# Kernel optimization log

Hardware: AMD Instinct MI355X
Metric: run time of the kernel (lower is better)

Reference implementation:

```python
import jax, jax.numpy as jnp
import numpy as np

B, L, D_T, DH, ALPHA, DTE, H, NL, DFF = 256, 64, 768, 128, 48, 64, 8, 3, 512


def setup_inputs() -> dict:
    key = jax.random.key(0)
    ks = jax.random.split(key, 24)
    n = lambda i, shape, s=1.0: jax.random.normal(ks[i], shape, dtype=jnp.float32) * s
    return {
        "cls_emb": n(0, (B, L, D_T)),
        "note_times": jnp.sort(jax.random.uniform(ks[1], (B, L), dtype=jnp.float32) * 48.0, axis=-1),
        "note_counts": jax.random.randint(ks[2], (B,), 1, L + 1).astype(jnp.int32),
        "proj_w": n(3, (D_T, DH), D_T ** -0.5), "proj_b": jnp.zeros((DH,), jnp.float32),
        "te_w": n(4, (DTE,)), "te_b": n(5, (DTE,)),
        "wq": n(6, (DTE, DTE), DTE ** -0.5), "wk": n(7, (DTE, DTE), DTE ** -0.5),
        "tf_wq": n(8, (NL, DH, DH), DH ** -0.5), "tf_wk": n(9, (NL, DH, DH), DH ** -0.5),
        "tf_wv": n(10, (NL, DH, DH), DH ** -0.5), "tf_wo": n(11, (NL, DH, DH), DH ** -0.5),
        "tf_ln1_g": jnp.ones((NL, DH), jnp.float32), "tf_ln1_b": jnp.zeros((NL, DH), jnp.float32),
        "tf_w1": n(12, (NL, DH, DFF), DH ** -0.5), "tf_b1": jnp.zeros((NL, DFF), jnp.float32),
        "tf_w2": n(13, (NL, DFF, DH), DFF ** -0.5), "tf_b2": jnp.zeros((NL, DH), jnp.float32),
        "tf_ln2_g": jnp.ones((NL, DH), jnp.float32), "tf_ln2_b": jnp.zeros((NL, DH), jnp.float32),
        "cls_w1": n(14, (DH, DH // 2), DH ** -0.5), "cls_b1": jnp.zeros((DH // 2,), jnp.float32),
        "cls_w2": n(15, (DH // 2, 1), (DH // 2) ** -0.5), "cls_b2": jnp.zeros((1,), jnp.float32),
    }


def _ln(x, g, b):
    mu = x.mean(-1, keepdims=True)
    var = x.var(-1, keepdims=True)
    return (x - mu) * jax.lax.rsqrt(var + 1e-5) * g + b


def _time_embed(t, w, b):
    # mTAND time embedding: dim 0 linear, rest periodic (sin)
    lin = t[..., None] * w + b
    return jnp.concatenate([lin[..., :1], jnp.sin(lin[..., 1:])], axis=-1)


def _forward(cls_emb, note_times, note_counts, proj_w, proj_b, te_w, te_b, wq, wk,
             tf_wq, tf_wk, tf_wv, tf_wo, tf_ln1_g, tf_ln1_b, tf_w1, tf_b1,
             tf_w2, tf_b2, tf_ln2_g, tf_ln2_b, cls_w1, cls_b1, cls_w2, cls_b2):
    # project frozen Longformer CLS embeddings -> note embeddings [B, L, DH]
    note_emb = cls_emb @ proj_w + proj_b
    alpha_pts = jnp.arange(ALPHA, dtype=jnp.float32)
    q_te = _time_embed(alpha_pts, te_w, te_b)          # [A, DTE]
    k_te = _time_embed(note_times, te_w, te_b)         # [B, L, DTE]
    dk = DTE // H
    q = (q_te @ wq).reshape(ALPHA, H, dk)
    k = (k_te @ wk).reshape(B, L, H, dk)
    scores = jnp.einsum('ahd,blhd->bhal', q, k) / np.float32(np.sqrt(dk))
    valid = jnp.arange(L)[None, :] < note_counts[:, None]      # [B, L] ragged mask
    scores = jnp.where(valid[:, None, None, :], scores, jnp.float32(-1e9))
    attn = jax.nn.softmax(scores, axis=-1)                     # [B, H, A, L]
    # one batched interpolation replaces the per-patient / per-dim python loops
    x = jnp.einsum('bhal,blf->bahf', attn, note_emb).mean(axis=2)  # [B, A, DH]
    x = jnp.where((note_counts > 0)[:, None, None], x, 0.0)
    # 3-layer post-norm transformer encoder over the alpha time grid
    hd = DH // H
    for i in range(NL):
        qh = (x @ tf_wq[i]).reshape(B, ALPHA, H, hd)
        kh = (x @ tf_wk[i]).reshape(B, ALPHA, H, hd)
        vh = (x @ tf_wv[i]).reshape(B, ALPHA, H, hd)
        s = jnp.einsum('bqhd,bkhd->bhqk', qh, kh) / np.float32(np.sqrt(hd))
        a = jax.nn.softmax(s, axis=-1)
        o = jnp.einsum('bhqk,bkhd->bqhd', a, vh).reshape(B, ALPHA, DH) @ tf_wo[i]
        x = _ln(x + o, tf_ln1_g[i], tf_ln1_b[i])
        f = jax.nn.relu(x @ tf_w1[i] + tf_b1[i]) @ tf_w2[i] + tf_b2[i]
        x = _ln(x + f, tf_ln2_g[i], tf_ln2_b[i])
    last = x[:, -1, :]
    logits = jax.nn.relu(last @ cls_w1 + cls_b1) @ cls_w2 + cls_b2
    return logits


def reference(cls_emb, note_times, note_counts, proj_w, proj_b, te_w, te_b, wq, wk,
              tf_wq, tf_wk, tf_wv, tf_wo, tf_ln1_g, tf_ln1_b, tf_w1, tf_b1,
              tf_w2, tf_b2, tf_ln2_g, tf_ln2_b, cls_w1, cls_b1, cls_w2, cls_b2):
    return _forward(cls_emb, note_times, note_counts, proj_w, proj_b, te_w, te_b, wq, wk,
                    tf_wq, tf_wk, tf_wv, tf_wo, tf_ln1_g, tf_ln1_b, tf_w1, tf_b1,
                    tf_w2, tf_b2, tf_ln2_g, tf_ln2_b, cls_w1, cls_b1, cls_w2, cls_b2)
```

## Files before the change

### kernel.cpp

```cpp
#include <hip/hip_runtime.h>
#include <hip/hip_bf16.h>

#define B_   256
#define L_   64
#define DT_  768
#define DH_  128
#define AL_  48
#define DTE_ 64
#define H_   8
#define NL_  3
#define DFF_ 512

typedef __attribute__((ext_vector_type(4))) float f32x4;
typedef __attribute__((ext_vector_type(4))) unsigned int u32x4;
typedef __attribute__((ext_vector_type(2))) unsigned int u32x2;
typedef __attribute__((ext_vector_type(8))) short short8;

__device__ inline unsigned short f2bf(float f) {
    union { float f; unsigned u; } v; v.f = f;
    unsigned r = (v.u + 0x7FFFu + ((v.u >> 16) & 1u)) >> 16;
    return (unsigned short)r;
}
__device__ inline unsigned f2bf2(float a, float b) {
    return (unsigned)f2bf(a) | ((unsigned)f2bf(b) << 16);
}
__device__ inline float bf2f(unsigned short u) {
    union { unsigned u; float f; } v; v.u = ((unsigned)u) << 16; return v.f;
}
__device__ inline short8 ldg8(const unsigned short* p) {
    union { short8 s; u32x4 v; } r;
    r.v = *(const u32x4*)p;
    return r.s;
}
__device__ inline unsigned pk_f16(float a, float b) {
    unsigned r;
    asm("v_cvt_pkrtz_f16_f32 %0, %1, %2" : "=v"(r) : "v"(a), "v"(b));
    return r;
}
__device__ inline unsigned pk_max(unsigned a, unsigned b) {
    unsigned r;
    asm("v_pk_max_f16 %0, %1, %2" : "=v"(r) : "v"(a), "v"(b));
    return r;
}
__device__ inline float f16_lo(unsigned h) {
    float f; asm("v_cvt_f32_f16 %0, %1" : "=v"(f) : "v"(h)); return f;
}
__device__ inline float f16_hi(unsigned h) {
    float f; unsigned t = h >> 16;
    asm("v_cvt_f32_f16 %0, %1" : "=v"(f) : "v"(t)); return f;
}

struct TEnt { const float* src; int dstOff; int K; int N; int tile0; };
struct TTab { TEnt e[19]; };

__global__ __launch_bounds__(256) void prep_weights_kernel(
    TTab tab, int ntile, unsigned short* __restrict__ wt,
    const float* __restrict__ te_w, const float* __restrict__ te_b,
    const float* __restrict__ wq, float* __restrict__ q_allG)
{
    __shared__ unsigned short lds[64][72];
    __shared__ float qte[AL_ * 68];
    int tid = threadIdx.x;
    if ((int)blockIdx.x >= ntile) {
        for (int i = tid; i < AL_ * 64; i += 256) {
            int a = i >> 6, j = i & 63;
            float lin = fmaf((float)a, te_w[j], te_b[j]);
            qte[a * 68 + j] = (j == 0) ? lin : __sinf(lin);
        }
        __syncthreads();
        for (int i = tid; i < AL_ * 64; i += 256) {
            int a = i >> 6, d = i & 63;
            float s0 = 0.f, s1 = 0.f, s2 = 0.f, s3 = 0.f;
            for (int j = 0; j < 64; j += 4) {
                s0 = fmaf(qte[a * 68 + j],     wq[j * 64 + d],       s0);
                s1 = fmaf(qte[a * 68 + j + 1], wq[(j + 1) * 64 + d], s1);
                s2 = fmaf(qte[a * 68 + j + 2], wq[(j + 2) * 64 + d], s2);
                s3 = fmaf(qte[a * 68 + j + 3], wq[(j + 3) * 64 + d], s3);
            }
            q_allG[i] = (s0 + s1) + (s2 + s3);
        }
        return;
    }
    int ei = 0;
    #pragma unroll
    for (int j = 1; j < 19; ++j) if ((int)blockIdx.x >= tab.e[j].tile0) ei = j;
    TEnt e = tab.e[ei];
    int t = blockIdx.x - e.tile0;
    int tilesK = e.K >> 6;
    int tk = t % tilesK, tn = t / tilesK;
    #pragma unroll
    for (int p = 0; p < 16; ++p) {
        int kk = p * 4 + (tid >> 6);
        int n = tid & 63;
        float v = e.src[(size_t)(tk * 64 + kk) * e.N + tn * 64 + n];
        lds[n][kk] = f2bf(v);
    }
    __syncthreads();
    #pragma unroll
    for (int p = 0; p < 2; ++p) {
        int c = p * 256 + tid;
        int n = c >> 3, q = c & 7;
        u32x4 v = *(const u32x4*)(&lds[n][q * 8]);
        *(u32x4*)(&wt[(size_t)e.dstOff + (size_t)(tn * 64 + n) * e.K + tk * 64 + q * 8]) = v;
    }
}

__global__ __launch_bounds__(256) void gemm_proj_kernel(
    const float* __restrict__ A, const unsigned short* __restrict__ Wt,
    const float* __restrict__ bias, unsigned short* __restrict__ C,
    int M, int N, int K)
{
    __shared__ unsigned short As[32 * 64];
    __shared__ unsigned short Bs[128 * 64];
    int tid = threadIdx.x;
    int bm = blockIdx.x * 32;
    int wave = tid >> 6, lane = tid & 63;
    int wm = wave >> 1, wn = wave & 1;
    int g = lane >> 4, r16 = lane & 15;

    f32x4 acc[4] = {};

    for (int k0 = 0; k0 < K; k0 += 64) {
        #pragma unroll
        for (int p = 0; p < 2; ++p) {
            int row = p * 16 + (tid >> 4);
            int c4 = tid & 15;
            f32x4 v = *(const f32x4*)(&A[(size_t)(bm + row) * K + k0 + c4 * 4]);
            u32x2 w;
            w[0] = f2bf2(v[0], v[1]);
            w[1] = f2bf2(v[2], v[3]);
            *(u32x2*)(&As[row * 64 + ((c4 * 4) ^ ((row & 7) << 3))]) = w;
        }
        #pragma unroll
        for (int p = 0; p < 4; ++p) {
            int c = p * 256 + tid;
            int n = c >> 3, q = c & 7;
            u32x4 v = *(const u32x4*)(&Wt[(size_t)n * K + k0 + q * 8]);
            *(u32x4*)(&Bs[n * 64 + ((q * 8) ^ ((n & 7) << 3))]) = v;
        }
        __syncthreads();
        #pragma unroll
        for (int kk = 0; kk < 2; ++kk) {
            short8 af, bf[4];
            int co = kk * 32 + g * 8;
            {
                int row = wm * 16 + r16;
                af = *(const short8*)(&As[row * 64 + (co ^ ((row & 7) << 3))]);
            }
            #pragma unroll
            for (int ni = 0; ni < 4; ++ni) {
                int row = wn * 64 + ni * 16 + r16;
                bf[ni] = *(const short8*)(&Bs[row * 64 + (co ^ ((row & 7) << 3))]);
            }
            #pragma unroll
            for (int ni = 0; ni < 4; ++ni)
                acc[ni] = __builtin_amdgcn_mfma_f32_16x16x32_bf16(af, bf[ni], acc[ni], 0, 0, 0);
        }
        __syncthreads();
    }
    #pragma unroll
    for (int ni = 0; ni < 4; ++ni) {
        int col = wn * 64 + ni * 16 + r16;
        float bv = bias[col];
        #pragma unroll
        for (int r = 0; r < 4; ++r) {
            int row = bm + wm * 16 + g * 4 + r;
            C[(size_t)row * N + col] = f2bf(acc[ni][r] + bv);
        }
    }
}

__global__ __launch_bounds__(256) void first_attn_kernel(
    const float* __restrict__ note_times, const int* __restrict__ note_counts,
    const float* __restrict__ te_w, const float* __restrict__ te_b,
    const float* __restrict__ wk, const float* __restrict__ q_all,
    const unsigned short* __restrict__ note_emb,
    float* __restrict__ x_out, unsigned short* __restrict__ xbf_out)
{
    __shared__ union RU {
        float kkL[64 * 68];
        unsigned short E[32 * 256];
        struct { unsigned short As[32 * 64]; unsigned short Bs[128 * 64]; } mm;
    } ru;
    __shared__ float rsL[32][8];

    const int bx = blockIdx.x;
    const int b = bx >> 1, a0 = (bx & 1) * 24;
    const int tid = threadIdx.x, lane = tid & 63;
    const int wv = __builtin_amdgcn_readfirstlane(tid >> 6);
    const int g = lane >> 4, r16 = lane & 15;
    const int nc = note_counts[b];

    float kte[64];
    {
        float t = note_times[b * 64 + lane];
        #pragma unroll
        for (int j = 0; j < 64; ++j) {
            float lin = fmaf(t, te_w[j], te_b[j]);
            kte[j] = (j == 0) ? lin : __sinf(lin);
        }
    }
    {
        float kvp[16] = {};
        #pragma unroll
        for (int j = 0; j < 64; ++j) {
            #pragma unroll
            for (int dd = 0; dd < 16; ++dd)
                kvp[dd] = fmaf(kte[j], wk[j * 64 + wv * 16 + dd], kvp[dd]);
        }
        #pragma unroll
        for (int q4 = 0; q4 < 4; ++q4)
            *(f32x4*)(&ru.kkL[lane * 68 + wv * 16 + q4 * 4]) = *(const f32x4*)(&kvp[q4 * 4]);
    }
    __syncthreads();
    float kv[64];
    #pragma unroll
    for (int q4 = 0; q4 < 16; ++q4)
        *(f32x4*)(&kv[q4 * 4]) = *(const f32x4*)(&ru.kkL[lane * 68 + q4 * 4]);
    __syncthreads();

    float abar[6] = {};
    const float scale = 0.35355339059327373f;
    #pragma unroll
    for (int p = 0; p < 2; ++p) {
        float e_reg[6][4];
        #pragma unroll
        for (int i = 0; i < 6; ++i) {
            int a = wv * 6 + i;
            float s[4];
            #pragma unroll
            for (int h = 0; h < 4; ++h) {
                float acc = 0.f;
                #pragma unroll
                for (int d = 0; d < 8; ++d)
                    acc = fmaf(q_all[(a0 + a) * 64 + p * 32 + h * 8 + d],
                               kv[p * 32 + h * 8 + d], acc);
                s[h] = (lane < nc) ? acc * scale : -1e9f;
            }
            unsigned m0 = pk_f16(s[0], s[1]);
            unsigned m1 = pk_f16(s[2], s[3]);
            #pragma unroll
            for (int st = 32; st >= 1; st >>= 1) {
                m0 = pk_max(m0, (unsigned)__shfl_xor((int)m0, st));
                m1 = pk_max(m1, (unsigned)__shfl_xor((int)m1, st));
            }
            float mm[4] = { f16_lo(m0), f16_hi(m0), f16_lo(m1), f16_hi(m1) };
            #pragma unroll
            for (int h = 0; h < 4; ++h) {
                float e = __expf(s[h] - mm[h]);
                e_reg[i][h] = e;
                int k = h * 64 + lane;
                ru.E[a * 256 + (k ^ ((a & 7) << 3))] = f2bf(e);
            }
        }
        __syncthreads();
        if (wv < 2) {
            f32x4 acc = {0.f, 0.f, 0.f, 0.f};
            #pragma unroll
            for (int ks = 0; ks < 8; ++ks) {
                int row = wv * 16 + r16;
                short8 af = *(const short8*)(&ru.E[row * 256 + ((ks * 32 + g * 8) ^ ((row & 7) << 3))]);
                short bb = (r16 == (ks >> 1)) ? (short)0x3F80 : (short)0;
                short8 bf = { bb, bb, bb, bb, bb, bb, bb, bb };
                acc = __builtin_amdgcn_mfma_f32_16x16x32_bf16(af, bf, acc, 0, 0, 0);
            }
            if (r16 < 4) {
                #pragma unroll
                for (int r = 0; r < 4; ++r)
                    rsL[wv * 16 + g * 4 + r][p * 4 + r16] = 0.125f / fmaxf(acc[r], 1e-20f);
            }
        }
        __syncthreads();
        #pragma unroll
        for (int i = 0; i < 6; ++i) {
            int a = wv * 6 + i;
            f32x4 rv = *(const f32x4*)(&rsL[a][p * 4]);
            abar[i] = fmaf(e_reg[i][0], rv[0], abar[i]);
            abar[i] = fmaf(e_reg[i][1], rv[1], abar[i]);
            abar[i] = fmaf(e_reg[i][2], rv[2], abar[i]);
            abar[i] = fmaf(e_reg[i][3], rv[3], abar[i]);
        }
    }
    {
        int l = tid & 63;
        #pragma unroll
        for (int pp = 0; pp < 4; ++pp) {
            int c = pp * 4 + (tid >> 6);
            u32x4 v = *(const u32x4*)(&note_emb[((size_t)b * 64 + l) * 128 + c * 8]);
            #pragma unroll
            for (int j = 0; j < 8; ++j) {
                unsigned short h16 = (unsigned short)((j & 1) ? (v[j >> 1] >> 16) : (v[j >> 1] & 0xffff));
                int f = c * 8 + j;
                ru.mm.Bs[f * 64 + (l ^ ((f & 7) << 3))] = h16;
            }
        }
    }
    #pragma unroll
    for (int i = 0; i < 6; ++i) {
        int a = wv * 6 + i;
        ru.mm.As[a * 64 + (lane ^ ((a & 7) << 3))] = f2bf(abar[i]);
    }
    __syncthreads();

    f32x4 pv[4] = {};
    #pragma unroll
    for (int q = 0; q < 4; ++q) {
        int f = wv * 4 + q, mi = f >> 3, ni = f & 7;
        #pragma unroll
        for (int ks = 0; ks < 2; ++ks) {
            int co = ks * 32 + g * 8;
            int raw = mi * 16 + r16, rb = ni * 16 + r16;
            short8 af = *(const short8*)(&ru.mm.As[raw * 64 + (co ^ ((raw & 7) << 3))]);
            short8 bf = *(const short8*)(&ru.mm.Bs[rb * 64 + (co ^ ((rb & 7) << 3))]);
            pv[q] = __builtin_amdgcn_mfma_f32_16x16x32_bf16(af, bf, pv[q], 0, 0, 0);
        }
    }
    #pragma unroll
    for (int q = 0; q < 4; ++q) {
        int f = wv * 4 + q, mi = f >> 3, ni = f & 7;
        #pragma unroll
        for (int r = 0; r < 4; ++r) {
            int row = mi * 16 + g * 4 + r;
            if (row < 24) {
                float v = (nc > 0) ? pv[q][r] : 0.f;
                size_t o = ((size_t)b * AL_ + a0 + row) * 128 + ni * 16 + r16;
                x_out[o] = v;
                xbf_out[o] = f2bf(v);
            }
        }
    }
}

__global__ __launch_bounds__(192) void attn2_kernel(
    const unsigned short* __restrict__ xbf, const unsigned short* __restrict__ WtL,
    unsigned short* __restrict__ o)
{
    __shared__ unsigned short Xs[AL_ * 128];
    __shared__ unsigned short qM[AL_ * 40];
    __shared__ unsigned short kM[AL_ * 40];
    __shared__ unsigned short vT[16 * 72];
    __shared__ float sL[AL_ * 52];
    __shared__ unsigned short P[AL_ * 64];
    int bid = blockIdx.x;
    int b = bid >> 3, h = bid & 7;
    int tid = threadIdx.x, lane = tid & 63;
    int wv = __builtin_amdgcn_readfirstlane(tid >> 6);
    int g = lane >> 4, r16 = lane & 15;

    #pragma unroll
    for (int p = 0; p < 4; ++p) {
        int i = p * 192 + tid;
        int a = i >> 4, c = (i & 15) * 8;
        u32x4 v = *(const u32x4*)(&xbf[((size_t)b * AL_ + a) * 128 + c]);
        *(u32x4*)(&Xs[a * 128 + (c & 64) + ((c & 63) ^ ((a & 7) << 3))]) = v;
    }
    for (int i = tid; i < 768; i += 192) {
        int a = i >> 4, k2 = 16 + (i & 15);
        qM[a * 40 + k2] = 0;
        kM[a * 40 + k2] = 0;
    }
    for (int i = tid; i < 256; i += 192) {
        int d = i >> 4, k2 = 48 + (i & 15);
        vT[d * 72 + k2] = 0;
    }
    for (int i = tid; i < 768; i += 192) {
        int a = i >> 4, c = 48 + (i & 15);
        P[a * 64 + (c ^ ((a & 7) << 3))] = 0;
    }
    __syncthreads();

    {
        f32x4 acc[3] = {};
        const unsigned short* Wm = WtL + wv * 16384 + (size_t)(h * 16) * 128;
        #pragma unroll
        for (int kq = 0; kq < 4; ++kq) {
            short8 bf = ldg8(&Wm[(size_t)r16 * 128 + kq * 32 + g * 8]);
            #pragma unroll
            for (int mi = 0; mi < 3; ++mi) {
                int row = mi * 16 + r16;
                int c = kq * 32 + g * 8;
                short8 af = *(const short8*)(&Xs[row * 128 + (c & 64) + ((c & 63) ^ ((row & 7) << 3))]);
                acc[mi] = __builtin_amdgcn_mfma_f32_16x16x32_bf16(af, bf, acc[mi], 0, 0, 0);
            }
        }
        #pragma unroll
        for (int mi = 0; mi < 3; ++mi) {
            #pragma unroll
            for (int r = 0; r < 4; ++r) {
                int a = mi * 16 + g * 4 + r;
                unsigned short hv = f2bf(acc[mi][r]);
                if (wv == 0) qM[a * 40 + r16] = hv;
                else if (wv == 1) kM[a * 40 + r16] = hv;
                else vT[r16 * 72 + a] = hv;
            }
        }
    }
    __syncthreads();

    {
        #pragma unroll
        for (int ni = 0; ni < 3; ++ni) {
            f32x4 acc = {0.f, 0.f, 0.f, 0.f};
            short8 af = *(const short8*)(&qM[(wv * 16 + r16) * 40 + g * 8]);
            short8 bf = *(const short8*)(&kM[(ni * 16 + r16) * 40 + g * 8]);
            acc = __builtin_amdgcn_mfma_f32_16x16x32_bf16(af, bf, acc, 0, 0, 0);
            #pragma unroll
            for (int r = 0; r < 4; ++r)
                sL[(wv * 16 + g * 4 + r) * 52 + ni * 16 + r16] = acc[r] * 0.25f;
        }
    }
    __syncthreads();

    {
        int row = wv * 16 + (lane >> 2), sub = lane & 3;
        f32x4 v0 = *(const f32x4*)(&sL[row * 52 + sub * 4]);
        f32x4 v1 = *(const f32x4*)(&sL[row * 52 + 16 + sub * 4]);
        f32x4 v2 = *(const f32x4*)(&sL[row * 52 + 32 + sub * 4]);
        float m = fmaxf(fmaxf(fmaxf(v0[0], v0[1]), fmaxf(v0[2], v0[3])),
                        fmaxf(fmaxf(v1[0], v1[1]), fmaxf(v1[2], v1[3])));
        m = fmaxf(m, fmaxf(fmaxf(v2[0], v2[1]), fmaxf(v2[2], v2[3])));
        m = fmaxf(m, __shfl_xor(m, 1));
        m = fmaxf(m, __shfl_xor(m, 2));
        float e[12];
        #pragma unroll
        for (int j = 0; j < 4; ++j) {
            e[j]     = __expf(v0[j] - m);
            e[4 + j] = __expf(v1[j] - m);
            e[8 + j] = __expf(v2[j] - m);
        }
        float sum = 0.f;
        #pragma unroll
        for (int j = 0; j < 12; ++j) sum += e[j];
        sum += __shfl_xor(sum, 1);
        sum += __shfl_xor(sum, 2);
        float inv = __fdividef(1.f, sum);
        #pragma unroll
        for (int c = 0; c < 3; ++c) {
            u32x2 w;
            w[0] = f2bf2(e[c * 4 + 0] * inv, e[c * 4 + 1] * inv);
            w[1] = f2bf2(e[c * 4 + 2] * inv, e[c * 4 + 3] * inv);
            int col = c * 16 + sub * 4;
            *(u32x2*)(&P[row * 64 + (col ^ ((row & 7) << 3))]) = w;
        }
    }
    __syncthreads();

    {
        f32x4 acc = {0.f, 0.f, 0.f, 0.f};
        #pragma unroll
        for (int ks = 0; ks < 2; ++ks) {
            int co = ks * 32 + g * 8;
            int rp = wv * 16 + r16;
            short8 af = *(const short8*)(&P[rp * 64 + (co ^ ((rp & 7) << 3))]);
            short8 bf = *(const short8*)(&vT[r16 * 72 + co]);
            acc = __builtin_amdgcn_mfma_f32_16x16x32_bf16(af, bf, acc, 0, 0, 0);
        }
        #pragma unroll
        for (int r = 0; r < 4; ++r) {
            int a = wv * 16 + g * 4 + r;
            o[((size_t)b * AL_ + a) * 128 + h * 16 + r16] = f2bf(acc[r]);
        }
    }
}

__global__ __launch_bounds__(256) void layer_tail_kernel(
    const unsigned short* __restrict__ obuf, const unsigned short* __restrict__ Wl,
    const float* __restrict__ b1, const float* __restrict__ b2,
    const float* __restrict__ g1, const float* __restrict__ be1,
    const float* __restrict__ g2, const float* __restrict__ be2,
    float* __restrict__ x, unsigned short* __restrict__ xbf,
    int last, const float* __restrict__ cw1, const float* __restrict__ cb1,
    const float* __restrict__ cw2, const float* __restrict__ cb2,
    float* __restrict__ outp)
{
    __shared__ unsigned short OX[16 * 128];
    __shared__ union { unsigned short hid[16 * 512]; float Cs[16 * 132]; } u2;
    __shared__ float xr[16 * 132];
    const int tid = threadIdx.x, lane = tid & 63;
    const int wv = __builtin_amdgcn_readfirstlane(tid >> 6);
    const int g = lane >> 4, r16 = lane & 15;
    const int row0 = last ? ((int)blockIdx.x * 48 + 32) : ((int)blockIdx.x * 16);

    {
        int a = tid >> 4, c = (tid & 15) * 8;
        u32x4 v = *(const u32x4*)(&obuf[(size_t)(row0 + a) * 128 + c]);
        *(u32x4*)(&OX[a * 128 + (c & 64) + ((c & 63) ^ ((a & 7) << 3))]) = v;
    }
    __syncthreads();

    {
        f32x4 wacc[2] = {};
        #pragma unroll
        for (int q = 0; q < 2; ++q) {
            int ni = wv * 2 + q;
            const unsigned short* Wm = Wl + 49152 + (size_t)(ni * 16 + r16) * 128;
            #pragma unroll
            for (int kq = 0; kq < 4; ++kq) {
                int co = kq * 32 + g * 8;
                short8 af = *(const short8*)(&OX[r16 * 128 + (co & 64) + ((co & 63) ^ ((r16 & 7) << 3))]);
                short8 bf = ldg8(Wm + co);
                wacc[q] = __builtin_amdgcn_mfma_f32_16x16x32_bf16(af, bf, wacc[q], 0, 0, 0);
            }
        }
        #pragma unroll
        for (int q = 0; q < 2; ++q) {
            int ni = wv * 2 + q;
            #pragma unroll
            for (int r = 0; r < 4; ++r)
                u2.Cs[(g * 4 + r) * 132 + ni * 16 + r16] = wacc[q][r];
        }
    }
    __syncthreads();

    #pragma unroll
    for (int rr = 0; rr < 4; ++rr) {
        int row = wv * 4 + rr;
        size_t go = (size_t)(row0 + row) * 128;
        float v0 = u2.Cs[row * 132 + lane] + x[go + lane];
        float v1 = u2.Cs[row * 132 + 64 + lane] + x[go + 64 + lane];
        float sum = v0 + v1, sq = v0 * v0 + v1 * v1;
        #pragma unroll
        for (int o2 = 32; o2 >= 1; o2 >>= 1) {
            sum += __shfl_xor(sum, o2);
            sq  += __shfl_xor(sq, o2);
        }
        float mu = sum * (1.f / 128.f);
        float var = sq * (1.f / 128.f) - mu * mu;
        float rs = rsqrtf(var + 1e-5f);
        float o0 = (v0 - mu) * rs * g1[lane] + be1[lane];
        float o1 = (v1 - mu) * rs * g1[lane + 64] + be1[lane + 64];
        xr[row * 132 + lane] = o0;
        xr[row * 132 + 64 + lane] = o1;
        OX[row * 128 + (lane ^ ((row & 7) << 3))] = f2bf(o0);
        OX[row * 128 + 64 + (lane ^ ((row & 7) << 3))] = f2bf(o1);
    }
    __syncthreads();

    {
        f32x4 hacc[8] = {};
        #pragma unroll
        for (int nf = 0; nf < 8; ++nf) {
            int col = wv * 128 + nf * 16 + r16;
            const unsigned short* Wm = Wl + 65536 + (size_t)col * 128;
            #pragma unroll
            for (int kq = 0; kq < 4; ++kq) {
                int co = kq * 32 + g * 8;
                short8 bf = ldg8(Wm + co);
                short8 af = *(const short8*)(&OX[r16 * 128 + (co & 64) + ((co & 63) ^ ((r16 & 7) << 3))]);
                hacc[nf] = __builtin_amdgcn_mfma_f32_16x16x32_bf16(af, bf, hacc[nf], 0, 0, 0);
            }
        }
        #pragma unroll
        for (int nf = 0; nf < 8; ++nf) {
            int col = wv * 128 + nf * 16 + r16;
            float bv = b1[col];
            #pragma unroll
            for (int r = 0; r < 4; ++r) {
                int rowa = g * 4 + r;
                u2.hid[rowa * 512 + (col & 448) + ((col & 63) ^ ((rowa & 7) << 3))] =
                    f2bf(fmaxf(hacc[nf][r] + bv, 0.f));
            }
        }
    }
    __syncthreads();

    f32x4 yacc[2] = {};
    #pragma unroll
    for (int q = 0; q < 2; ++q) {
        int ni = wv * 2 + q;
        const unsigned short* Wm = Wl + 131072 + (size_t)(ni * 16 + r16) * 512;
        #pragma unroll
        for (int kq = 0; kq < 16; ++kq) {
            int co = kq * 32 + g * 8;
            short8 af = *(const short8*)(&u2.hid[r16 * 512 + (co & 448) + ((co & 63) ^ ((r16 & 7) << 3))]);
            short8 bf = ldg8(Wm + co);
            yacc[q] = __builtin_amdgcn_mfma_f32_16x16x32_bf16(af, bf, yacc[q], 0, 0, 0);
        }
    }
    __syncthreads();
    #pragma unroll
    for (int q = 0; q < 2; ++q) {
        int ni = wv * 2 + q;
        float bv = b2[ni * 16 + r16];
        #pragma unroll
        for (int r = 0; r < 4; ++r)
            u2.Cs[(g * 4 + r) * 132 + ni * 16 + r16] = yacc[q][r] + bv;
    }
    __syncthreads();

    #pragma unroll
    for (int rr = 0; rr < 4; ++rr) {
        int row = wv * 4 + rr;
        size_t go = (size_t)(row0 + row) * 128;
        float v0 = u2.Cs[row * 132 + lane] + xr[row * 132 + lane];
        float v1 = u2.Cs[row * 132 + 64 + lane] + xr[row * 132 + 64 + lane];
        float sum = v0 + v1, sq = v0 * v0 + v1 * v1;
        #pragma unroll
        for (int o2 = 32; o2 >= 1; o2 >>= 1) {
            sum += __shfl_xor(sum, o2);
            sq  += __shfl_xor(sq, o2);
        }
        float mu = sum * (1.f / 128.f);
        float var = sq * (1.f / 128.f) - mu * mu;
        float rs = rsqrtf(var + 1e-5f);
        float o0 = (v0 - mu) * rs * g2[lane] + be2[lane];
        float o1 = (v1 - mu) * rs * g2[lane + 64] + be2[lane + 64];
        if (!last) {
            x[go + lane] = o0;
            x[go + 64 + lane] = o1;
            xbf[go + lane] = f2bf(o0);
            xbf[go + 64 + lane] = f2bf(o1);
        } else {
            xr[row * 132 + lane] = o0;
            xr[row * 132 + 64 + lane] = o1;
        }
    }
    if (last) {
        __syncthreads();
        if (wv == 0) {
            float hj = cb1[lane];
            #pragma unroll 8
            for (int d = 0; d < 128; ++d)
                hj = fmaf(xr[15 * 132 + d], cw1[d * 64 + lane], hj);
            hj = fmaxf(hj, 0.f);
            float acc = hj * cw2[lane];
            #pragma unroll
            for (int o2 = 32; o2 >= 1; o2 >>= 1) acc += __shfl_xor(acc, o2);
            if (lane == 0) outp[blockIdx.x] = acc + cb2[0];
        }
    }
}

extern "C" void kernel_launch(void* const* d_in, const int* in_sizes, int n_in,
                              void* d_out, int out_size, void* d_ws, size_t ws_size,
                              hipStream_t stream) {
    (void)in_sizes; (void)n_in; (void)out_size; (void)ws_size;
    const float* cls_emb    = (const float*)d_in[0];
    const float* note_times = (const float*)d_in[1];
    const int*   note_counts= (const int*)d_in[2];
    const float* proj_w     = (const float*)d_in[3];
    const float* proj_b     = (const float*)d_in[4];
    const float* te_w       = (const float*)d_in[5];
    const float* te_b       = (const float*)d_in[6];
    const float* wq         = (const float*)d_in[7];
    const float* wk         = (const float*)d_in[8];
    const float* tf_wq      = (const float*)d_in[9];
    const float* tf_wk      = (const float*)d_in[10];
    const float* tf_wv      = (const float*)d_in[11];
    const float* tf_wo      = (const float*)d_in[12];
    const float* tf_ln1_g   = (const float*)d_in[13];
    const float* tf_ln1_b   = (const float*)d_in[14];
    const float* tf_w1      = (const float*)d_in[15];
    const float* tf_b1      = (const float*)d_in[16];
    const float* tf_w2      = (const float*)d_in[17];
    const float* tf_b2      = (const float*)d_in[18];
    const float* tf_ln2_g   = (const float*)d_in[19];
    const float* tf_ln2_b   = (const float*)d_in[20];
    const float* cls_w1     = (const float*)d_in[21];
    const float* cls_b1     = (const float*)d_in[22];
    const float* cls_w2     = (const float*)d_in[23];
    const float* cls_b2     = (const float*)d_in[24];
    float* out = (float*)d_out;
    float* ws = (float*)d_ws;

    unsigned short* note_emb16 = (unsigned short*)(ws + 0);
    float* x        = ws + 1048576;
    unsigned short* obuf16 = (unsigned short*)(ws + 2621440);
    unsigned short* xbf    = (unsigned short*)(ws + 3407872);
    float* q_all    = ws + 4194304;
    unsigned short* wt     = (unsigned short*)(ws + 4197376);

    TTab tab;
    int tile = 0, idx = 0;
    auto add = [&](const float* src, int dstOff, int K, int N) {
        tab.e[idx].src = src; tab.e[idx].dstOff = dstOff;
        tab.e[idx].K = K; tab.e[idx].N = N; tab.e[idx].tile0 = tile;
        tile += (K / 64) * (N / 64); ++idx;
    };
    add(proj_w, 0, DT_, DH_);
    int layerBase[NL_];
    for (int i = 0; i < NL_; ++i) {
        int base = 98304 + i * 196608;
        layerBase[i] = base;
        add(tf_wq + (size_t)i * DH_ * DH_, base,           DH_, DH_);
        add(tf_wk + (size_t)i * DH_ * DH_, base + 16384,   DH_, DH_);
        add(tf_wv + (size_t)i * DH_ * DH_, base + 32768,   DH_, DH_);
        add(tf_wo + (size_t)i * DH_ * DH_, base + 49152,   DH_, DH_);
        add(tf_w1 + (size_t)i * DH_ * DFF_, base + 65536,  DH_, DFF_);
        add(tf_w2 + (size_t)i * DFF_ * DH_, base + 131072, DFF_, DH_);
    }
    prep_weights_kernel<<<tile + 1, 256, 0, stream>>>(tab, tile, wt, te_w, te_b, wq, q_all);

    const int Mx = B_ * AL_;

    gemm_proj_kernel<<<(B_ * L_) / 32, 256, 0, stream>>>(
        cls_emb, wt, proj_b, note_emb16, B_ * L_, DH_, DT_);

    first_attn_kernel<<<B_ * 2, 256, 0, stream>>>(
        note_times, note_counts, te_w, te_b, wk, q_all, note_emb16, x, xbf);

    for (int i = 0; i < NL_; ++i) {
        int base = layerBase[i];
        int last = (i == NL_ - 1);
        attn2_kernel<<<B_ * H_, 192, 0, stream>>>(xbf, wt + base, obuf16);
        layer_tail_kernel<<<last ? B_ : (Mx / 16), 256, 0, stream>>>(
            obuf16, wt + base,
            tf_b1 + i * DFF_, tf_b2 + i * DH_,
            tf_ln1_g + i * DH_, tf_ln1_b + i * DH_,
            tf_ln2_g + i * DH_, tf_ln2_b + i * DH_,
            x, xbf,
            last, cls_w1, cls_b1, cls_w2, cls_b2, out);
    }
}
```

Before: 187.5 us.

## Process 32 rows per layer-tail block and alias attention shared buffers

The layer tail kernel is templated on the number of rows per block. Non-final layers now use 32-row tiles, so each loaded weight fragment feeds two MFMA row tiles and global weight traffic per row is halved. The attention kernel overlays its shared buffers through unions: X with the score buffer, and the q/k buffers with P, with P's zero padding moved to after the softmax. This is meant to cut LDS footprint and raise occupancy, at the cost of more registers and fewer blocks in the tail kernel.

After: 174.0 us. 1.08x faster.

```diff
diff --git a/kernel.cpp b/kernel.cpp
--- a/kernel.cpp
+++ b/kernel.cpp
@@ -335,12 +335,15 @@
     const unsigned short* __restrict__ xbf, const unsigned short* __restrict__ WtL,
     unsigned short* __restrict__ o)
 {
-    __shared__ unsigned short Xs[AL_ * 128];
-    __shared__ unsigned short qM[AL_ * 40];
-    __shared__ unsigned short kM[AL_ * 40];
+    __shared__ union UA {
+        unsigned short Xs[AL_ * 128];
+        float sL[AL_ * 52];
+    } ua;
+    __shared__ union UB {
+        struct { unsigned short qM[AL_ * 40]; unsigned short kM[AL_ * 40]; } qk;
+        unsigned short P[AL_ * 64];
+    } ub;
     __shared__ unsigned short vT[16 * 72];
-    __shared__ float sL[AL_ * 52];
-    __shared__ unsigned short P[AL_ * 64];
     int bid = blockIdx.x;
     int b = bid >> 3, h = bid & 7;
     int tid = threadIdx.x, lane = tid & 63;
@@ -352,21 +355,17 @@
         int i = p * 192 + tid;
         int a = i >> 4, c = (i & 15) * 8;
         u32x4 v = *(const u32x4*)(&xbf[((size_t)b * AL_ + a) * 128 + c]);
-        *(u32x4*)(&Xs[a * 128 + (c & 64) + ((c & 63) ^ ((a & 7) << 3))]) = v;
+        *(u32x4*)(&ua.Xs[a * 128 + (c & 64) + ((c & 63) ^ ((a & 7) << 3))]) = v;
     }
     for (int i = tid; i < 768; i += 192) {
         int a = i >> 4, k2 = 16 + (i & 15);
-        qM[a * 40 + k2] = 0;
-        kM[a * 40 + k2] = 0;
+        ub.qk.qM[a * 40 + k2] = 0;
+        ub.qk.kM[a * 40 + k2] = 0;
     }
     for (int i = tid; i < 256; i += 192) {
         int d = i >> 4, k2 = 48 + (i & 15);
         vT[d * 72 + k2] = 0;
     }
-    for (int i = tid; i < 768; i += 192) {
-        int a = i >> 4, c = 48 + (i & 15);
-        P[a * 64 + (c ^ ((a & 7) << 3))] = 0;
-    }
     __syncthreads();
 
     {
@@ -379,7 +378,7 @@
             for (int mi = 0; mi < 3; ++mi) {
                 int row = mi * 16 + r16;
                 int c = kq * 32 + g * 8;
-                short8 af = *(const short8*)(&Xs[row * 128 + (c & 64) + ((c & 63) ^ ((row & 7) << 3))]);
+                short8 af = *(const short8*)(&ua.Xs[row * 128 + (c & 64) + ((c & 63) ^ ((row & 7) << 3))]);
                 acc[mi] = __builtin_amdgcn_mfma_f32_16x16x32_bf16(af, bf, acc[mi], 0, 0, 0);
             }
         }
@@ -389,8 +388,8 @@
             for (int r = 0; r < 4; ++r) {
                 int a = mi * 16 + g * 4 + r;
                 unsigned short hv = f2bf(acc[mi][r]);
-                if (wv == 0) qM[a * 40 + r16] = hv;
-                else if (wv == 1) kM[a * 40 + r16] = hv;
+                if (wv == 0) ub.qk.qM[a * 40 + r16] = hv;
+                else if (wv == 1) ub.qk.kM[a * 40 + r16] = hv;
                 else vT[r16 * 72 + a] = hv;
             }
         }
@@ -401,21 +400,21 @@
         #pragma unroll
         for (int ni = 0; ni < 3; ++ni) {
             f32x4 acc = {0.f, 0.f, 0.f, 0.f};
-            short8 af = *(const short8*)(&qM[(wv * 16 + r16) * 40 + g * 8]);
-            short8 bf = *(const short8*)(&kM[(ni * 16 + r16) * 40 + g * 8]);
+            short8 af = *(const short8*)(&ub.qk.qM[(wv * 16 + r16) * 40 + g * 8]);
+            short8 bf = *(const short8*)(&ub.qk.kM[(ni * 16 + r16) * 40 + g * 8]);
             acc = __builtin_amdgcn_mfma_f32_16x16x32_bf16(af, bf, acc, 0, 0, 0);
             #pragma unroll
             for (int r = 0; r < 4; ++r)
-                sL[(wv * 16 + g * 4 + r) * 52 + ni * 16 + r16] = acc[r] * 0.25f;
+                ua.sL[(wv * 16 + g * 4 + r) * 52 + ni * 16 + r16] = acc[r] * 0.25f;
         }
     }
     __syncthreads();
 
     {
         int row = wv * 16 + (lane >> 2), sub = lane & 3;
-        f32x4 v0 = *(const f32x4*)(&sL[row * 52 + sub * 4]);
-        f32x4 v1 = *(const f32x4*)(&sL[row * 52 + 16 + sub * 4]);
-        f32x4 v2 = *(const f32x4*)(&sL[row * 52 + 32 + sub * 4]);
+        f32x4 v0 = *(const f32x4*)(&ua.sL[row * 52 + sub * 4]);
+        f32x4 v1 = *(const f32x4*)(&ua.sL[row * 52 + 16 + sub * 4]);
+        f32x4 v2 = *(const f32x4*)(&ua.sL[row * 52 + 32 + sub * 4]);
         float m = fmaxf(fmaxf(fmaxf(v0[0], v0[1]), fmaxf(v0[2], v0[3])),
                         fmaxf(fmaxf(v1[0], v1[1]), fmaxf(v1[2], v1[3])));
         m = fmaxf(m, fmaxf(fmaxf(v2[0], v2[1]), fmaxf(v2[2], v2[3])));
@@ -440,7 +439,11 @@
             w[0] = f2bf2(e[c * 4 + 0] * inv, e[c * 4 + 1] * inv);
             w[1] = f2bf2(e[c * 4 + 2] * inv, e[c * 4 + 3] * inv);
             int col = c * 16 + sub * 4;
-            *(u32x2*)(&P[row * 64 + (col ^ ((row & 7) << 3))]) = w;
+            *(u32x2*)(&ub.P[row * 64 + (col ^ ((row & 7) << 3))]) = w;
+        }
+        for (int i = tid; i < 768; i += 192) {
+            int a = i >> 4, c = 48 + (i & 15);
+            ub.P[a * 64 + (c ^ ((a & 7) << 3))] = 0;
         }
     }
     __syncthreads();
@@ -451,7 +454,7 @@
         for (int ks = 0; ks < 2; ++ks) {
             int co = ks * 32 + g * 8;
             int rp = wv * 16 + r16;
-            short8 af = *(const short8*)(&P[rp * 64 + (co ^ ((rp & 7) << 3))]);
+            short8 af = *(const short8*)(&ub.P[rp * 64 + (co ^ ((rp & 7) << 3))]);
             short8 bf = *(const short8*)(&vT[r16 * 72 + co]);
             acc = __builtin_amdgcn_mfma_f32_16x16x32_bf16(af, bf, acc, 0, 0, 0);
         }
@@ -463,6 +466,7 @@
     }
 }
 
+template<int ROWS>
 __global__ __launch_bounds__(256) void layer_tail_kernel(
     const unsigned short* __restrict__ obuf, const unsigned short* __restrict__ Wl,
     const float* __restrict__ b1, const float* __restrict__ b2,
@@ -473,23 +477,26 @@
     const float* __restrict__ cw2, const float* __restrict__ cb2,
     float* __restrict__ outp)
 {
-    __shared__ unsigned short OX[16 * 128];
-    __shared__ union { unsigned short hid[16 * 512]; float Cs[16 * 132]; } u2;
-    __shared__ float xr[16 * 132];
+    constexpr int MR = ROWS / 16;
+    __shared__ unsigned short OX[ROWS * 128];
+    __shared__ union { unsigned short hid[ROWS * 512]; float Cs[ROWS * 132]; } u2;
+    __shared__ float xr[ROWS * 132];
     const int tid = threadIdx.x, lane = tid & 63;
     const int wv = __builtin_amdgcn_readfirstlane(tid >> 6);
     const int g = lane >> 4, r16 = lane & 15;
-    const int row0 = last ? ((int)blockIdx.x * 48 + 32) : ((int)blockIdx.x * 16);
-
-    {
-        int a = tid >> 4, c = (tid & 15) * 8;
+    const int row0 = last ? ((int)blockIdx.x * 48 + 32) : ((int)blockIdx.x * ROWS);
+
+    #pragma unroll
+    for (int p = 0; p < MR; ++p) {
+        int i = p * 256 + tid;
+        int a = i >> 4, c = (i & 15) * 8;
         u32x4 v = *(const u32x4*)(&obuf[(size_t)(row0 + a) * 128 + c]);
         *(u32x4*)(&OX[a * 128 + (c & 64) + ((c & 63) ^ ((a & 7) << 3))]) = v;
     }
     __syncthreads();
 
     {
-        f32x4 wacc[2] = {};
+        f32x4 wacc[MR][2] = {};
         #pragma unroll
         for (int q = 0; q < 2; ++q) {
             int ni = wv * 2 + q;
@@ -497,24 +504,30 @@
             #pragma unroll
             for (int kq = 0; kq < 4; ++kq) {
                 int co = kq * 32 + g * 8;
-                short8 af = *(const short8*)(&OX[r16 * 128 + (co & 64) + ((co & 63) ^ ((r16 & 7) << 3))]);
                 short8 bf = ldg8(Wm + co);
-                wacc[q] = __builtin_amdgcn_mfma_f32_16x16x32_bf16(af, bf, wacc[q], 0, 0, 0);
-            }
-        }
-        #pragma unroll
-        for (int q = 0; q < 2; ++q) {
-            int ni = wv * 2 + q;
-            #pragma unroll
-            for (int r = 0; r < 4; ++r)
-                u2.Cs[(g * 4 + r) * 132 + ni * 16 + r16] = wacc[q][r];
-        }
-    }
-    __syncthreads();
-
-    #pragma unroll
-    for (int rr = 0; rr < 4; ++rr) {
-        int row = wv * 4 + rr;
+                #pragma unroll
+                for (int mi = 0; mi < MR; ++mi) {
+                    int ra = mi * 16 + r16;
+                    short8 af = *(const short8*)(&OX[ra * 128 + (co & 64) + ((co & 63) ^ ((ra & 7) << 3))]);
+                    wacc[mi][q] = __builtin_amdgcn_mfma_f32_16x16x32_bf16(af, bf, wacc[mi][q], 0, 0, 0);
+                }
+            }
+        }
+        #pragma unroll
+        for (int mi = 0; mi < MR; ++mi)
+            #pragma unroll
+            for (int q = 0; q < 2; ++q) {
+                int ni = wv * 2 + q;
+                #pragma unroll
+                for (int r = 0; r < 4; ++r)
+                    u2.Cs[(mi * 16 + g * 4 + r) * 132 + ni * 16 + r16] = wacc[mi][q][r];
+            }
+    }
+    __syncthreads();
+
+    #pragma unroll
+    for (int rr = 0; rr < ROWS / 4; ++rr) {
+        int row = wv * (ROWS / 4) + rr;
         size_t go = (size_t)(row0 + row) * 128;
         float v0 = u2.Cs[row * 132 + lane] + x[go + lane];
         float v1 = u2.Cs[row * 132 + 64 + lane] + x[go + 64 + lane];
@@ -537,7 +550,7 @@
     __syncthreads();
 
     {
-        f32x4 hacc[8] = {};
+        f32x4 hacc[MR][8] = {};
         #pragma unroll
         for (int nf = 0; nf < 8; ++nf) {
             int col = wv * 128 + nf * 16 + r16;
@@ -546,8 +559,12 @@
             for (int kq = 0; kq < 4; ++kq) {
                 int co = kq * 32 + g * 8;
                 short8 bf = ldg8(Wm + co);
-                short8 af = *(const short8*)(&OX[r16 * 128 + (co & 64) + ((co & 63) ^ ((r16 & 7) << 3))]);
-                hacc[nf] = __builtin_amdgcn_mfma_f32_16x16x32_bf16(af, bf, hacc[nf], 0, 0, 0);
+                #pragma unroll
+                for (int mi = 0; mi < MR; ++mi) {
+                    int ra = mi * 16 + r16;
+                    short8 af = *(const short8*)(&OX[ra * 128 + (co & 64) + ((co & 63) ^ ((ra & 7) << 3))]);
+                    hacc[mi][nf] = __builtin_amdgcn_mfma_f32_16x16x32_bf16(af, bf, hacc[mi][nf], 0, 0, 0);
+                }
             }
         }
         #pragma unroll
@@ -555,16 +572,18 @@
             int col = wv * 128 + nf * 16 + r16;
             float bv = b1[col];
             #pragma unroll
-            for (int r = 0; r < 4; ++r) {
-                int rowa = g * 4 + r;
-                u2.hid[rowa * 512 + (col & 448) + ((col & 63) ^ ((rowa & 7) << 3))] =
-                    f2bf(fmaxf(hacc[nf][r] + bv, 0.f));
-            }
-        }
-    }
-    __syncthreads();
-
-    f32x4 yacc[2] = {};
+            for (int mi = 0; mi < MR; ++mi)
+                #pragma unroll
+                for (int r = 0; r < 4; ++r) {
+                    int rowa = mi * 16 + g * 4 + r;
+                    u2.hid[rowa * 512 + (col & 448) + ((col & 63) ^ ((rowa & 7) << 3))] =
+                        f2bf(fmaxf(hacc[mi][nf][r] + bv, 0.f));
+                }
+        }
+    }
+    __syncthreads();
+
+    f32x4 yacc[MR][2] = {};
     #pragma unroll
     for (int q = 0; q < 2; ++q) {
         int ni = wv * 2 + q;
@@ -572,25 +591,31 @@
         #pragma unroll
         for (int kq = 0; kq < 16; ++kq) {
             int co = kq * 32 + g * 8;
-            short8 af = *(const short8*)(&u2.hid[r16 * 512 + (co & 448) + ((co & 63) ^ ((r16 & 7) << 3))]);
             short8 bf = ldg8(Wm + co);
-            yacc[q] = __builtin_amdgcn_mfma_f32_16x16x32_bf16(af, bf, yacc[q], 0, 0, 0);
-        }
-    }
-    __syncthreads();
-    #pragma unroll
-    for (int q = 0; q < 2; ++q) {
-        int ni = wv * 2 + q;
-        float bv = b2[ni * 16 + r16];
-        #pragma unroll
-        for (int r = 0; r < 4; ++r)
-            u2.Cs[(g * 4 + r) * 132 + ni * 16 + r16] = yacc[q][r] + bv;
-    }
-    __syncthreads();
-
-    #pragma unroll
-    for (int rr = 0; rr < 4; ++rr) {
-        int row = wv * 4 + rr;
+            #pragma unroll
+            for (int mi = 0; mi < MR; ++mi) {
+                int ra = mi * 16 + r16;
+                short8 af = *(const short8*)(&u2.hid[ra * 512 + (co & 448) + ((co & 63) ^ ((ra & 7) << 3))]);
+                yacc[mi][q] = __builtin_amdgcn_mfma_f32_16x16x32_bf16(af, bf, yacc[mi][q], 0, 0, 0);
+            }
+        }
+    }
+    __syncthreads();
+    #pragma unroll
+    for (int mi = 0; mi < MR; ++mi)
+        #pragma unroll
+        for (int q = 0; q < 2; ++q) {
+            int ni = wv * 2 + q;
+            float bv = b2[ni * 16 + r16];
+            #pragma unroll
+            for (int r = 0; r < 4; ++r)
+                u2.Cs[(mi * 16 + g * 4 + r) * 132 + ni * 16 + r16] = yacc[mi][q][r] + bv;
+        }
+    __syncthreads();
+
+    #pragma unroll
+    for (int rr = 0; rr < ROWS / 4; ++rr) {
+        int row = wv * (ROWS / 4) + rr;
         size_t go = (size_t)(row0 + row) * 128;
         float v0 = u2.Cs[row * 132 + lane] + xr[row * 132 + lane];
         float v1 = u2.Cs[row * 132 + 64 + lane] + xr[row * 132 + 64 + lane];
@@ -621,7 +646,7 @@
             float hj = cb1[lane];
             #pragma unroll 8
             for (int d = 0; d < 128; ++d)
-                hj = fmaf(xr[15 * 132 + d], cw1[d * 64 + lane], hj);
+                hj = fmaf(xr[(ROWS - 1) * 132 + d], cw1[d * 64 + lane], hj);
             hj = fmaxf(hj, 0.f);
             float acc = hj * cw2[lane];
             #pragma unroll
@@ -703,12 +728,22 @@
         int base = layerBase[i];
         int last = (i == NL_ - 1);
         attn2_kernel<<<B_ * H_, 192, 0, stream>>>(xbf, wt + base, obuf16);
-        layer_tail_kernel<<<last ? B_ : (Mx / 16), 256, 0, stream>>>(
-            obuf16, wt + base,
-            tf_b1 + i * DFF_, tf_b2 + i * DH_,
-            tf_ln1_g + i * DH_, tf_ln1_b + i * DH_,
-            tf_ln2_g + i * DH_, tf_ln2_b + i * DH_,
-            x, xbf,
-            last, cls_w1, cls_b1, cls_w2, cls_b2, out);
-    }
-}
+        if (!last) {
+            layer_tail_kernel<32><<<Mx / 32, 256, 0, stream>>>(
+                obuf16, wt + base,
+                tf_b1 + i * DFF_, tf_b2 + i * DH_,
+                tf_ln1_g + i * DH_, tf_ln1_b + i * DH_,
+                tf_ln2_g + i * DH_, tf_ln2_b + i * DH_,
+                x, xbf,
+                0, cls_w1, cls_b1, cls_w2, cls_b2, out);
+        } else {
+            layer_tail_kernel<16><<<B_, 256, 0, stream>>>(
+                obuf16, wt + base,
+                tf_b1 + i * DFF_, tf_b2 + i * DH_,
+                tf_ln1_g + i * DH_, tf_ln1_b + i * DH_,
+                tf_ln2_g + i * DH_, tf_ln2_b + i * DH_,
+                x, xbf,
+                1, cls_w1, cls_b1, cls_w2, cls_b2, out);
+        }
+    }
+}
```
